# Performance work log

Hardware: AMD Instinct MI355X
Metric: run time of the kernel (lower is better)

Reference implementation:

```python
import jax, jax.numpy as jnp
import numpy as np

D = 256      # embedding_dim
DI = 512     # inner dim = proj_factor * D
H = 4        # num heads
DH = DI // H # head dim
L = 4        # num blocks
K = 4        # causal conv kernel size

def _ln(x, g, b):
    mu = jnp.mean(x, -1, keepdims=True)
    v = jnp.var(x, -1, keepdims=True)
    return (x - mu) * jax.lax.rsqrt(v + 1e-5) * g + b

def _causal_conv(x, w, b):
    # x [B,S,DI], w [K,DI] depthwise causal conv
    S = x.shape[1]
    xp = jnp.pad(x, ((0, 0), (K - 1, 0), (0, 0)))
    out = b
    for j in range(K):
        out = out + xp[:, j:j + S, :] * w[j]
    return out

def _mlstm(q, k, v, ip, fp):
    # parallel stabilized mLSTM. q,k,v [B,S,H,DH]; ip,fp [B,S,H]
    q = q.transpose(0, 2, 1, 3)
    k = k.transpose(0, 2, 1, 3)
    v = v.transpose(0, 2, 1, 3)
    ip = ip.transpose(0, 2, 1)  # [B,H,S]
    fp = fp.transpose(0, 2, 1)
    lf = jax.nn.log_sigmoid(fp)                      # log forget gates
    Fc = jnp.cumsum(lf, axis=-1)
    Fc = jnp.concatenate([jnp.zeros_like(Fc[..., :1]), Fc], axis=-1)  # [B,H,S+1]
    logfg = Fc[..., 1:, None] - Fc[..., None, 1:]    # [B,H,S,S]: sum of log f over (s,t]
    S_len = q.shape[2]
    tri = jnp.tril(jnp.ones((S_len, S_len), dtype=bool))
    logD = jnp.where(tri, logfg + ip[..., None, :], jnp.float32(-1e30))
    m = jnp.max(logD, axis=-1, keepdims=True)        # stabilizer
    Dm = jnp.exp(logD - m)
    qk = jnp.einsum('bhtd,bhsd->bhts', q, k) * (DH ** -0.5)
    C = qk * Dm
    norm = jnp.maximum(jnp.abs(jnp.sum(C, axis=-1, keepdims=True)), jnp.exp(-m))
    h = jnp.einsum('bhts,bhsd->bhtd', C / (norm + 1e-6), v)
    return h.transpose(0, 2, 1, 3)

def _forward(x, time_features, Wp, bp, ln_g, ln_b, Wup, bup, conv_w, conv_b,
             Wq, Wk, Wv, Wif, bif, gn_g, gn_b, skip, Wdown, bdown,
             lnf_g, lnf_b, Wf, bf):
    B, S = x.shape
    xi = jnp.concatenate([x[..., None], time_features], axis=-1)  # [B,S,5]
    h = xi @ Wp + bp                                              # [B,S,D]
    for l in range(L):
        res = h
        hn = _ln(h, ln_g[l], ln_b[l])
        up = hn @ Wup[l] + bup[l]                 # [B,S,2*DI]
        xm, z = up[..., :DI], up[..., DI:]
        xc = jax.nn.silu(_causal_conv(xm, conv_w[l], conv_b[l]))
        q = (xc @ Wq[l]).reshape(B, S, H, DH)
        k = (xc @ Wk[l]).reshape(B, S, H, DH)
        v = (xm @ Wv[l]).reshape(B, S, H, DH)
        gi = jnp.concatenate([q.reshape(B, S, DI), k.reshape(B, S, DI), v.reshape(B, S, DI)], axis=-1)
        gates = gi @ Wif[l] + bif[l]              # [B,S,2H]
        ht = _mlstm(q, k, v, gates[..., :H], gates[..., H:])  # [B,S,H,DH]
        ht = _ln(ht, gn_g[l].reshape(H, DH), gn_b[l].reshape(H, DH)).reshape(B, S, DI)
        ht = ht + skip[l] * xc
        ht = ht * jax.nn.silu(z)
        h = res + ht @ Wdown[l] + bdown[l]
    h = _ln(h, lnf_g, lnf_b)
    return h[:, -1, :] @ Wf + bf                  # [B,1]

def setup_inputs():
    key = jax.random.key(0)
    ks = jax.random.split(key, 16)
    B, S = 8, 1024
    sd = jnp.float32(0.02)
    return {
        'x': jax.random.normal(ks[0], (B, S), jnp.float32),
        'time_features': jax.random.normal(ks[1], (B, S, 4), jnp.float32),
        'Wp': jax.random.normal(ks[2], (5, D)) * sd, 'bp': jnp.zeros((D,)),
        'ln_g': jnp.ones((L, D)), 'ln_b': jnp.zeros((L, D)),
        'Wup': jax.random.normal(ks[3], (L, D, 2 * DI)) * sd, 'bup': jnp.zeros((L, 2 * DI)),
        'conv_w': jax.random.normal(ks[4], (L, K, DI)) * sd, 'conv_b': jnp.zeros((L, DI)),
        'Wq': jax.random.normal(ks[5], (L, DI, DI)) * sd,
        'Wk': jax.random.normal(ks[6], (L, DI, DI)) * sd,
        'Wv': jax.random.normal(ks[7], (L, DI, DI)) * sd,
        'Wif': jax.random.normal(ks[8], (L, 3 * DI, 2 * H)) * sd, 'bif': jnp.zeros((L, 2 * H)),
        'gn_g': jnp.ones((L, DI)), 'gn_b': jnp.zeros((L, DI)),
        'skip': jnp.ones((L, DI)),
        'Wdown': jax.random.normal(ks[9], (L, DI, D)) * sd, 'bdown': jnp.zeros((L, D)),
        'lnf_g': jnp.ones((D,)), 'lnf_b': jnp.zeros((D,)),
        'Wf': jax.random.normal(ks[10], (D, 1)) * sd, 'bf': jnp.zeros((1,)),
    }

def reference(x, time_features, Wp, bp, ln_g, ln_b, Wup, bup, conv_w, conv_b,
              Wq, Wk, Wv, Wif, bif, gn_g, gn_b, skip, Wdown, bdown,
              lnf_g, lnf_b, Wf, bf):
    return _forward(x, time_features, Wp, bp, ln_g, ln_b, Wup, bup, conv_w, conv_b,
                    Wq, Wk, Wv, Wif, bif, gn_g, gn_b, skip, Wdown, bdown,
                    lnf_g, lnf_b, Wf, bf)
```

## Files before the change

### kernel.cpp

```cpp
#include <hip/hip_runtime.h>
#include <hip/hip_bf16.h>
#include <math.h>

#define S 1024
#define NLAYER 4

typedef __bf16 bf16x8 __attribute__((ext_vector_type(8)));
typedef float floatx4 __attribute__((ext_vector_type(4)));

__device__ __forceinline__ float wave_sum(float v) {
  #pragma unroll
  for (int off = 32; off > 0; off >>= 1) v += __shfl_xor(v, off, 64);
  return v;
}

__device__ __forceinline__ void wtrans_body(
    int bid, const float* Wup, const float* Wq, const float* Wk, const float* Wv,
    const float* Wdown, __bf16* WupT, __bf16* WqkT, __bf16* WvT, __bf16* WdownT) {
  __shared__ float T[32][33];
  int layer = bid / 1152, rr = bid % 1152;
  const float* src; __bf16* dst; int K, N, tile;
  if (rr < 256)       { src = Wup   + layer * 262144; dst = WupT  + layer * 262144;          K = 256; N = 1024; tile = rr; }
  else if (rr < 512)  { src = Wq    + layer * 262144; dst = WqkT  + layer * 524288;          K = 512; N = 512;  tile = rr - 256; }
  else if (rr < 768)  { src = Wk    + layer * 262144; dst = WqkT  + layer * 524288 + 262144; K = 512; N = 512;  tile = rr - 512; }
  else if (rr < 1024) { src = Wv    + layer * 262144; dst = WvT   + layer * 262144;          K = 512; N = 512;  tile = rr - 768; }
  else                { src = Wdown + layer * 131072; dst = WdownT + layer * 131072;         K = 512; N = 256;  tile = rr - 1024; }
  int ntn = N >> 5;
  int tk = tile / ntn, tn = tile % ntn;
  int tid = threadIdx.x;
  int r = tid >> 3, c4 = (tid & 7) * 4;
  float4 v = *(const float4*)(src + (size_t)(tk * 32 + r) * N + tn * 32 + c4);
  T[c4 + 0][r] = v.x; T[c4 + 1][r] = v.y; T[c4 + 2][r] = v.z; T[c4 + 3][r] = v.w;
  __syncthreads();
  __bf16 o[4];
  #pragma unroll
  for (int j = 0; j < 4; ++j) o[j] = (__bf16)T[r][c4 + j];
  *(uint2*)(dst + (size_t)(tn * 32 + r) * K + tk * 32 + c4) = *(uint2*)o;
}

__device__ __forceinline__ void wgprep_body(
    int bid, const float* Wq, const float* Wk, const float* Wv,
    const float* Wif, float* wg) {
  int l = bid >> 8;
  int rem = bid & 255;
  int sel = rem >> 7;
  int kg = rem & 127;
  int tid = threadIdx.x;
  int wv = tid >> 6, lane = tid & 63;
  int k = kg * 4 + wv;
  const float* wif = Wif + (size_t)l * 1536 * 8;
  float part[8] = {0, 0, 0, 0, 0, 0, 0, 0};
  if (sel == 0) {
    const float* qr = Wq + (size_t)l * 262144 + (size_t)k * 512;
    const float* kr = Wk + (size_t)l * 262144 + (size_t)k * 512;
    #pragma unroll
    for (int i = 0; i < 8; ++i) {
      int n = lane + i * 64;
      float qv = qr[n], kv = kr[n];
      const float* wq8 = wif + (size_t)n * 8;
      const float* wk8 = wif + (size_t)(512 + n) * 8;
      #pragma unroll
      for (int j = 0; j < 8; ++j) part[j] += qv * wq8[j] + kv * wk8[j];
    }
  } else {
    const float* vr = Wv + (size_t)l * 262144 + (size_t)k * 512;
    #pragma unroll
    for (int i = 0; i < 8; ++i) {
      int n = lane + i * 64;
      float vv = vr[n];
      const float* wv8 = wif + (size_t)(1024 + n) * 8;
      #pragma unroll
      for (int j = 0; j < 8; ++j) part[j] += vv * wv8[j];
    }
  }
  #pragma unroll
  for (int j = 0; j < 8; ++j) part[j] = wave_sum(part[j]);
  if (lane < 8) wg[(size_t)l * 8192 + sel * 4096 + (size_t)k * 8 + lane] = part[lane];
}

__device__ __forceinline__ void embed_body(
    int row, const float* x, const float* tf, const float* Wp, const float* bp,
    const float* g, const float* b, float* h, __bf16* hn) {
  int n = threadIdx.x;
  float xv = x[row];
  const float* t4 = tf + (size_t)row * 4;
  float acc = bp[n] + xv * Wp[n];
  acc += t4[0] * Wp[256 + n];
  acc += t4[1] * Wp[512 + n];
  acc += t4[2] * Wp[768 + n];
  acc += t4[3] * Wp[1024 + n];
  h[(size_t)row * 256 + n] = acc;
  __shared__ float red[4];
  int wid = n >> 6, lane = n & 63;
  float s = wave_sum(acc);
  if (lane == 0) red[wid] = s;
  __syncthreads();
  float mu = (red[0] + red[1] + red[2] + red[3]) * (1.f / 256.f);
  __syncthreads();
  float d = acc - mu;
  float s2 = wave_sum(d * d);
  if (lane == 0) red[wid] = s2;
  __syncthreads();
  float var = (red[0] + red[1] + red[2] + red[3]) * (1.f / 256.f);
  float rs = rsqrtf(var + 1e-5f);
  hn[(size_t)row * 256 + n] = (__bf16)(d * rs * g[n] + b[n]);
}

__global__ __launch_bounds__(256) void prep_kernel(
    const float* __restrict__ x, const float* __restrict__ tf,
    const float* __restrict__ Wp, const float* __restrict__ bp,
    const float* __restrict__ ln_g, const float* __restrict__ ln_b,
    const float* __restrict__ Wup, const float* __restrict__ Wq,
    const float* __restrict__ Wk, const float* __restrict__ Wv,
    const float* __restrict__ Wdown, const float* __restrict__ Wif,
    __bf16* __restrict__ WupT, __bf16* __restrict__ WqkT,
    __bf16* __restrict__ WvT, __bf16* __restrict__ WdownT,
    float* __restrict__ wg, float* __restrict__ h, __bf16* __restrict__ hn) {
  int bid = blockIdx.x;
  if (bid < 4608) {
    wtrans_body(bid, Wup, Wq, Wk, Wv, Wdown, WupT, WqkT, WvT, WdownT);
  } else if (bid < 4608 + 1024) {
    wgprep_body(bid - 4608, Wq, Wk, Wv, Wif, wg);
  } else {
    embed_body(bid - 5632, x, tf, Wp, bp, ln_g, ln_b, h, hn);
  }
}

template <int TM, int MODE, int ACC>
__device__ __forceinline__ void hgemm_body(
    char* smem_raw,
    const __bf16* __restrict__ A, int lda,
    const __bf16* __restrict__ BT, int Kdim,
    const float* __restrict__ bias,
    void* __restrict__ Cout, int ldc, int bxi, int byi) {
  auto As = (__bf16(*)[40])smem_raw;
  auto Bs = (__bf16(*)[40])(smem_raw + (size_t)TM * 80);
  int tid = threadIdx.x;
  int bm = bxi * TM, bn = byi * 128;
  int wid = tid >> 6, lane = tid & 63;
  int wr = wid >> 1, wc = wid & 1;
  int lg = lane >> 4, li = lane & 15;
  constexpr int MI = TM / 32;
  constexpr int WROW = TM / 2;
  floatx4 acc[MI][4];
  #pragma unroll
  for (int i = 0; i < MI; ++i)
    #pragma unroll
    for (int j = 0; j < 4; ++j) acc[i][j] = (floatx4)(0.f);

  int arow = tid >> 2, aseg = tid & 3;
  bf16x8 pa0, pa1, pb0, pb1;
  auto pre = [&](int k0) {
    pa0 = *(const bf16x8*)(A + (size_t)(bm + arow) * lda + k0 + aseg * 8);
    if constexpr (TM == 128)
      pa1 = *(const bf16x8*)(A + (size_t)(bm + arow + 64) * lda + k0 + aseg * 8);
    pb0 = *(const bf16x8*)(BT + (size_t)(bn + arow) * Kdim + k0 + aseg * 8);
    pb1 = *(const bf16x8*)(BT + (size_t)(bn + arow + 64) * Kdim + k0 + aseg * 8);
  };
  pre(0);
  for (int k0 = 0; k0 < Kdim; k0 += 32) {
    __syncthreads();
    *(bf16x8*)&As[arow][aseg * 8] = pa0;
    if constexpr (TM == 128) *(bf16x8*)&As[arow + 64][aseg * 8] = pa1;
    *(bf16x8*)&Bs[arow][aseg * 8] = pb0;
    *(bf16x8*)&Bs[arow + 64][aseg * 8] = pb1;
    __syncthreads();
    if (k0 + 32 < Kdim) pre(k0 + 32);
    bf16x8 af[MI], bfr[4];
    #pragma unroll
    for (int mi = 0; mi < MI; ++mi)
      af[mi] = *(const bf16x8*)&As[wr * WROW + mi * 16 + li][lg * 8];
    #pragma unroll
    for (int ni = 0; ni < 4; ++ni)
      bfr[ni] = *(const bf16x8*)&Bs[wc * 64 + ni * 16 + li][lg * 8];
    #pragma unroll
    for (int mi = 0; mi < MI; ++mi)
      #pragma unroll
      for (int ni = 0; ni < 4; ++ni)
        acc[mi][ni] = __builtin_amdgcn_mfma_f32_16x16x32_bf16(af[mi], bfr[ni], acc[mi][ni], 0, 0, 0);
  }
  if constexpr (MODE == 1) {
    __bf16* eb = (__bf16*)smem_raw;
    const int PITCH = 136;
    __bf16* C = (__bf16*)Cout;
    #pragma unroll
    for (int mi = 0; mi < MI; ++mi) {
      __syncthreads();
      #pragma unroll
      for (int ni = 0; ni < 4; ++ni) {
        int col = wc * 64 + ni * 16 + li;
        float bz = bias ? bias[bn + col] : 0.f;
        #pragma unroll
        for (int r = 0; r < 4; ++r) {
          int lr = wr * 16 + lg * 4 + r;
          eb[lr * PITCH + col] = (__bf16)(acc[mi][ni][r] + bz);
        }
      }
      __syncthreads();
      #pragma unroll
      for (int i = 0; i < 2; ++i) {
        int lr = (tid >> 4) + i * 16;
        int c8 = (tid & 15) * 8;
        bf16x8 v = *(const bf16x8*)&eb[lr * PITCH + c8];
        int row_g = bm + (lr >> 4) * 64 + mi * 16 + (lr & 15);
        *(bf16x8*)(C + (size_t)row_g * ldc + bn + c8) = v;
      }
    }
  } else {
    #pragma unroll
    for (int mi = 0; mi < MI; ++mi) {
      int row = bm + wr * WROW + mi * 16 + lg * 4;
      #pragma unroll
      for (int ni = 0; ni < 4; ++ni) {
        int col = bn + wc * 64 + ni * 16 + li;
        if constexpr (MODE == 2) {
          __bf16 o4[4];
          #pragma unroll
          for (int r = 0; r < 4; ++r) o4[r] = (__bf16)acc[mi][ni][r];
          __bf16* vt = (__bf16*)Cout;
          size_t off = ((size_t)((row >> 10) * 4 + (col >> 7)) * 128 + (col & 127)) * 1024 + (row & 1023);
          *(uint2*)(vt + off) = *(uint2*)o4;
        } else {
          float bz = bias ? bias[col] : 0.f;
          float* C = (float*)Cout;
          #pragma unroll
          for (int r = 0; r < 4; ++r) {
            float v = acc[mi][ni][r] + bz;
            if (ACC) v += C[(size_t)(row + r) * ldc + col];
            C[(size_t)(row + r) * ldc + col] = v;
          }
        }
      }
    }
  }
}

template <int TM, int MODE, int ACC>
__global__ __launch_bounds__(256) void hgemm(
    const __bf16* __restrict__ A, int lda,
    const __bf16* __restrict__ BT, int Kdim,
    const float* __restrict__ bias,
    void* __restrict__ Cout, int ldc) {
  extern __shared__ char smem[];
  hgemm_body<TM, MODE, ACC>(smem, A, lda, BT, Kdim, bias, Cout, ldc,
                            blockIdx.x, blockIdx.y);
}

__global__ __launch_bounds__(256) void qkv_kernel(
    const __bf16* __restrict__ xc, const __bf16* __restrict__ WqkT,
    __bf16* __restrict__ qk, const __bf16* __restrict__ up,
    const __bf16* __restrict__ WvT, __bf16* __restrict__ vT) {
  extern __shared__ char smem[];
  if (blockIdx.y < 8) {
    hgemm_body<128, 1, 0>(smem, xc, 512, WqkT, 512, nullptr, qk, 1024,
                          blockIdx.x, blockIdx.y);
  } else {
    int j = blockIdx.y - 8;
    hgemm_body<64, 2, 0>(smem, up, 1024, WvT, 512, nullptr, vT, 0,
                         blockIdx.x * 2 + (j & 1), j >> 1);
  }
}

__global__ __launch_bounds__(256) void dgemm_ln_kernel(
    const __bf16* __restrict__ A, const __bf16* __restrict__ BT,
    const float* __restrict__ bias, float* __restrict__ h,
    const float* __restrict__ lng, const float* __restrict__ lnb,
    __bf16* __restrict__ hn) {
  __shared__ __bf16 As[32][40];
  __shared__ __bf16 Bs[256][40];
  __shared__ float redS[2][32], redQ[2][32];
  int tid = threadIdx.x;
  int bm = blockIdx.x * 32;
  int wid = tid >> 6, lane = tid & 63;
  int wr = wid >> 1, wc = wid & 1;
  int lg = lane >> 4, li = lane & 15;
  floatx4 acc[8];
  #pragma unroll
  for (int j = 0; j < 8; ++j) acc[j] = (floatx4)(0.f);

  int arow = tid >> 2, aseg = tid & 3;
  bf16x8 pa, pb[4];
  auto pre = [&](int k0) {
    if (tid < 128)
      pa = *(const bf16x8*)(A + (size_t)(bm + arow) * 512 + k0 + aseg * 8);
    #pragma unroll
    for (int i = 0; i < 4; ++i)
      pb[i] = *(const bf16x8*)(BT + (size_t)(arow + i * 64) * 512 + k0 + aseg * 8);
  };
  pre(0);
  for (int k0 = 0; k0 < 512; k0 += 32) {
    __syncthreads();
    if (tid < 128) *(bf16x8*)&As[arow][aseg * 8] = pa;
    #pragma unroll
    for (int i = 0; i < 4; ++i) *(bf16x8*)&Bs[arow + i * 64][aseg * 8] = pb[i];
    __syncthreads();
    if (k0 + 32 < 512) pre(k0 + 32);
    bf16x8 af = *(const bf16x8*)&As[wr * 16 + li][lg * 8];
    #pragma unroll
    for (int ni = 0; ni < 8; ++ni) {
      bf16x8 bfr = *(const bf16x8*)&Bs[wc * 128 + ni * 16 + li][lg * 8];
      acc[ni] = __builtin_amdgcn_mfma_f32_16x16x32_bf16(af, bfr, acc[ni], 0, 0, 0);
    }
  }
  #pragma unroll
  for (int r = 0; r < 4; ++r) {
    int lr = wr * 16 + lg * 4 + r;
    int row = bm + lr;
    float s1 = 0.f, s2 = 0.f;
    #pragma unroll
    for (int ni = 0; ni < 8; ++ni) {
      int col = wc * 128 + ni * 16 + li;
      float v = acc[ni][r] + bias[col] + h[(size_t)row * 256 + col];
      acc[ni][r] = v;
      h[(size_t)row * 256 + col] = v;
      s1 += v;
      s2 += v * v;
    }
    s1 += __shfl_xor(s1, 1, 64); s1 += __shfl_xor(s1, 2, 64);
    s1 += __shfl_xor(s1, 4, 64); s1 += __shfl_xor(s1, 8, 64);
    s2 += __shfl_xor(s2, 1, 64); s2 += __shfl_xor(s2, 2, 64);
    s2 += __shfl_xor(s2, 4, 64); s2 += __shfl_xor(s2, 8, 64);
    if (li == 0) { redS[wc][lr] = s1; redQ[wc][lr] = s2; }
  }
  if (!lng) return;
  __syncthreads();
  #pragma unroll
  for (int r = 0; r < 4; ++r) {
    int lr = wr * 16 + lg * 4 + r;
    int row = bm + lr;
    float s1 = redS[0][lr] + redS[1][lr];
    float s2 = redQ[0][lr] + redQ[1][lr];
    float mu = s1 * (1.f / 256.f);
    float var = s2 * (1.f / 256.f) - mu * mu;
    float rs = rsqrtf(var + 1e-5f);
    #pragma unroll
    for (int ni = 0; ni < 8; ++ni) {
      int col = wc * 128 + ni * 16 + li;
      hn[(size_t)row * 256 + col] = (__bf16)((acc[ni][r] - mu) * rs * lng[col] + lnb[col]);
    }
  }
}

__global__ __launch_bounds__(256) void conv_silu_kernel(
    const __bf16* __restrict__ up, const float* __restrict__ cw,
    const float* __restrict__ cb, const float* __restrict__ wg,
    const float* __restrict__ bif, __bf16* __restrict__ xc,
    float* __restrict__ gates) {
  int tid = threadIdx.x;
  int wv = tid >> 6, lane = tid & 63;
  int row = blockIdx.x * 4 + wv;
  int c8 = lane * 8;
  int t = row & (S - 1);
  float acc[8];
  *(float4*)&acc[0] = *(const float4*)(cb + c8);
  *(float4*)&acc[4] = *(const float4*)(cb + c8 + 4);
  float xm[8];
  #pragma unroll
  for (int j = 0; j < 4; ++j) {
    int tt = t - 3 + j;
    if (tt >= 0) {
      bf16x8 xv = *(const bf16x8*)(up + (size_t)(row - 3 + j) * 1024 + c8);
      float4 w0 = *(const float4*)(cw + j * 512 + c8);
      float4 w1 = *(const float4*)(cw + j * 512 + c8 + 4);
      acc[0] += w0.x * (float)xv[0]; acc[1] += w0.y * (float)xv[1];
      acc[2] += w0.z * (float)xv[2]; acc[3] += w0.w * (float)xv[3];
      acc[4] += w1.x * (float)xv[4]; acc[5] += w1.y * (float)xv[5];
      acc[6] += w1.z * (float)xv[6]; acc[7] += w1.w * (float)xv[7];
      if (j == 3) {
        #pragma unroll
        for (int m = 0; m < 8; ++m) xm[m] = (float)xv[m];
      }
    }
  }
  bf16x8 o;
  float xcs[8];
  #pragma unroll
  for (int m = 0; m < 8; ++m) {
    float sg = 1.f / (1.f + __expf(-acc[m]));
    xcs[m] = acc[m] * sg;
    o[m] = (__bf16)xcs[m];
  }
  *(bf16x8*)(xc + (size_t)row * 512 + c8) = o;
  const float* w1 = wg + (size_t)c8 * 8;
  const float* w2 = wg + 4096 + (size_t)c8 * 8;
  float part[8] = {0, 0, 0, 0, 0, 0, 0, 0};
  #pragma unroll
  for (int m = 0; m < 8; ++m) {
    const float* a = w1 + m * 8;
    const float* b = w2 + m * 8;
    #pragma unroll
    for (int j = 0; j < 8; ++j) part[j] += xcs[m] * a[j] + xm[m] * b[j];
  }
  #pragma unroll
  for (int j = 0; j < 8; ++j) part[j] = wave_sum(part[j]);
  if (lane < 8) gates[(size_t)row * 8 + lane] = part[lane] + bif[lane];
}

__global__ __launch_bounds__(64) void scan_kernel(
    const float* __restrict__ gates, float* __restrict__ gout,
    float* __restrict__ Mout, float* __restrict__ NFout) {
  int bh = blockIdx.x;
  int bb = bh >> 2, hh = bh & 3;
  int lane = threadIdx.x;
  float ip[16], pf[16];
  #pragma unroll
  for (int i = 0; i < 16; ++i) {
    int t = lane * 16 + i;
    const float* grow = gates + ((size_t)(bb * S + t)) * 8;
    ip[i] = grow[hh];
    float fp = grow[4 + hh];
    float lf = fminf(fp, 0.f) - log1pf(__expf(-fabsf(fp)));
    pf[i] = (i == 0) ? lf : pf[i - 1] + lf;
  }
  float T = pf[15];
  float inc = T;
  #pragma unroll
  for (int off = 1; off < 64; off <<= 1) {
    float v = __shfl_up(inc, off, 64);
    if (lane >= off) inc += v;
  }
  float excl = inc - T;
  float F[16], g[16], pm[16];
  #pragma unroll
  for (int i = 0; i < 16; ++i) {
    F[i] = excl + pf[i];
    g[i] = ip[i] - F[i];
    pm[i] = (i == 0) ? g[0] : fmaxf(pm[i - 1], g[i]);
  }
  float Mx = pm[15];
  float incm = Mx;
  #pragma unroll
  for (int off = 1; off < 64; off <<= 1) {
    float v = __shfl_up(incm, off, 64);
    if (lane >= off) incm = fmaxf(incm, v);
  }
  float em = __shfl_up(incm, 1, 64);
  if (lane == 0) em = -3.4e38f;
  #pragma unroll
  for (int i = 0; i < 16; ++i) {
    int t = lane * 16 + i;
    size_t o = (size_t)bh * S + t;
    float M = fmaxf(em, pm[i]);
    gout[o] = g[i];
    Mout[o] = M;
    NFout[o] = __expf(-F[i] - M);
  }
}

__global__ __launch_bounds__(256, 1) void attn_kernel(
    const __bf16* __restrict__ qk, const __bf16* __restrict__ vT,
    const float* __restrict__ gbuf, const float* __restrict__ Mbuf,
    const float* __restrict__ NFbuf,
    const float* __restrict__ gn_g, const float* __restrict__ gn_b,
    const float* __restrict__ skip,
    const __bf16* __restrict__ xc, const __bf16* __restrict__ up,
    __bf16* __restrict__ hd) {
  __shared__ __bf16 Ks[64][136];
  __shared__ __bf16 Vs[128][72];
  __shared__ __bf16 plds[4][2][16][72];
  __shared__ float gls[64];
  __shared__ float glds[128], blds[128], slds[128];
  int px = blockIdx.y, bh = blockIdx.x;
  int tqA = px, tqB = 15 - px;
  int bb = bh >> 2, hh = bh & 3;
  int tid = threadIdx.x;
  int wv = tid >> 6, lane = tid & 63;
  int lg = lane >> 4, li = lane & 15;
  int tbA = tqA * 64 + wv * 16;
  int tbB = tqB * 64 + wv * 16;
  const float scale = 0.08838834764831845f;

  if (tid < 128) {
    glds[tid] = gn_g[hh * 128 + tid];
    blds[tid] = gn_b[hh * 128 + tid];
    slds[tid] = skip[hh * 128 + tid];
  }

  bf16x8 aqA[4], aqB[4];
  {
    const __bf16* qpA = qk + ((size_t)(bb * S + tbA + li)) * 1024 + hh * 128 + lg * 8;
    const __bf16* qpB = qk + ((size_t)(bb * S + tbB + li)) * 1024 + hh * 128 + lg * 8;
    #pragma unroll
    for (int cd = 0; cd < 4; ++cd) {
      aqA[cd] = *(const bf16x8*)(qpA + cd * 32);
      aqB[cd] = *(const bf16x8*)(qpB + cd * 32);
    }
  }
  float mlA[4], nfA[4], mlB[4], nfB[4];
  #pragma unroll
  for (int r = 0; r < 4; ++r) {
    mlA[r] = Mbuf[(size_t)bh * S + tbA + lg * 4 + r];
    nfA[r] = NFbuf[(size_t)bh * S + tbA + lg * 4 + r];
    mlB[r] = Mbuf[(size_t)bh * S + tbB + lg * 4 + r];
    nfB[r] = NFbuf[(size_t)bh * S + tbB + lg * 4 + r];
  }

  floatx4 oA[8], oB[8];
  #pragma unroll
  for (int df = 0; df < 8; ++df) { oA[df] = (floatx4)(0.f); oB[df] = (floatx4)(0.f); }
  float rsA[4] = {0, 0, 0, 0}, rsB[4] = {0, 0, 0, 0};

  int krow = tid >> 3, kcol = tid & 7;
  bf16x8 kreg[4], vreg[4];
  float greg = 0.f;
  auto preload = [&](int st) {
    int s0 = st * 64;
    const __bf16* kp = qk + ((size_t)(bb * S + s0 + krow)) * 1024 + 512 + hh * 128;
    kreg[0] = *(const bf16x8*)(kp + kcol * 8);
    kreg[1] = *(const bf16x8*)(kp + (size_t)32 * 1024 + kcol * 8);
    kreg[2] = *(const bf16x8*)(kp + 64 + kcol * 8);
    kreg[3] = *(const bf16x8*)(kp + (size_t)32 * 1024 + 64 + kcol * 8);
    #pragma unroll
    for (int i = 0; i < 4; ++i)
      vreg[i] = *(const bf16x8*)(vT + ((size_t)(bh * 128 + krow + i * 32)) * 1024 + s0 + kcol * 8);
    if (tid < 64) greg = gbuf[(size_t)bh * S + s0 + tid];
  };
  preload(0);

  for (int st = 0; st <= tqB; ++st) {
    __syncthreads();
    *(bf16x8*)&Ks[krow][kcol * 8] = kreg[0];
    *(bf16x8*)&Ks[krow + 32][kcol * 8] = kreg[1];
    *(bf16x8*)&Ks[krow][64 + kcol * 8] = kreg[2];
    *(bf16x8*)&Ks[krow + 32][64 + kcol * 8] = kreg[3];
    #pragma unroll
    for (int i = 0; i < 4; ++i) *(bf16x8*)&Vs[krow + i * 32][kcol * 8] = vreg[i];
    if (tid < 64) gls[tid] = greg;
    __syncthreads();
    if (st < tqB) preload(st + 1);

    int s0 = st * 64;
    bool actA = (st <= tqA);
    #pragma unroll
    for (int ns = 0; ns < 4; ++ns) {
      bf16x8 bk0 = *(const bf16x8*)&Ks[ns * 16 + li][lg * 8];
      bf16x8 bk1 = *(const bf16x8*)&Ks[ns * 16 + li][32 + lg * 8];
      bf16x8 bk2 = *(const bf16x8*)&Ks[ns * 16 + li][64 + lg * 8];
      bf16x8 bk3 = *(const bf16x8*)&Ks[ns * 16 + li][96 + lg * 8];
      int s = s0 + ns * 16 + li;
      float gv = gls[ns * 16 + li];
      if (actA) {
        floatx4 pa = (floatx4)(0.f);
        pa = __builtin_amdgcn_mfma_f32_16x16x32_bf16(aqA[0], bk0, pa, 0, 0, 0);
        pa = __builtin_amdgcn_mfma_f32_16x16x32_bf16(aqA[1], bk1, pa, 0, 0, 0);
        pa = __builtin_amdgcn_mfma_f32_16x16x32_bf16(aqA[2], bk2, pa, 0, 0, 0);
        pa = __builtin_amdgcn_mfma_f32_16x16x32_bf16(aqA[3], bk3, pa, 0, 0, 0);
        #pragma unroll
        for (int r = 0; r < 4; ++r) {
          int t = tbA + lg * 4 + r;
          float val = pa[r] * scale * __expf(gv - mlA[r]);
          float w = (s <= t) ? val : 0.f;
          rsA[r] += w;
          plds[wv][0][lg * 4 + r][ns * 16 + li] = (__bf16)w;
        }
      }
      {
        floatx4 pb = (floatx4)(0.f);
        pb = __builtin_amdgcn_mfma_f32_16x16x32_bf16(aqB[0], bk0, pb, 0, 0, 0);
        pb = __builtin_amdgcn_mfma_f32_16x16x32_bf16(aqB[1], bk1, pb, 0, 0, 0);
        pb = __builtin_amdgcn_mfma_f32_16x16x32_bf16(aqB[2], bk2, pb, 0, 0, 0);
        pb = __builtin_amdgcn_mfma_f32_16x16x32_bf16(aqB[3], bk3, pb, 0, 0, 0);
        #pragma unroll
        for (int r = 0; r < 4; ++r) {
          int t = tbB + lg * 4 + r;
          float val = pb[r] * scale * __expf(gv - mlB[r]);
          float w = (s <= t) ? val : 0.f;
          rsB[r] += w;
          plds[wv][1][lg * 4 + r][ns * 16 + li] = (__bf16)w;
        }
      }
    }
    bf16x8 apA0, apA1, apB0, apB1;
    if (actA) {
      apA0 = *(const bf16x8*)&plds[wv][0][li][lg * 8];
      apA1 = *(const bf16x8*)&plds[wv][0][li][32 + lg * 8];
    }
    apB0 = *(const bf16x8*)&plds[wv][1][li][lg * 8];
    apB1 = *(const bf16x8*)&plds[wv][1][li][32 + lg * 8];
    #pragma unroll
    for (int df = 0; df < 8; ++df) {
      bf16x8 bv0 = *(const bf16x8*)&Vs[df * 16 + li][lg * 8];
      bf16x8 bv1 = *(const bf16x8*)&Vs[df * 16 + li][32 + lg * 8];
      if (actA) {
        oA[df] = __builtin_amdgcn_mfma_f32_16x16x32_bf16(apA0, bv0, oA[df], 0, 0, 0);
        oA[df] = __builtin_amdgcn_mfma_f32_16x16x32_bf16(apA1, bv1, oA[df], 0, 0, 0);
      }
      oB[df] = __builtin_amdgcn_mfma_f32_16x16x32_bf16(apB0, bv0, oB[df], 0, 0, 0);
      oB[df] = __builtin_amdgcn_mfma_f32_16x16x32_bf16(apB1, bv1, oB[df], 0, 0, 0);
    }
  }
  #pragma unroll
  for (int r = 0; r < 4; ++r) {
    float a = rsA[r], b = rsB[r];
    a += __shfl_xor(a, 1, 64); a += __shfl_xor(a, 2, 64);
    a += __shfl_xor(a, 4, 64); a += __shfl_xor(a, 8, 64);
    b += __shfl_xor(b, 1, 64); b += __shfl_xor(b, 2, 64);
    b += __shfl_xor(b, 4, 64); b += __shfl_xor(b, 8, 64);
    rsA[r] = a; rsB[r] = b;
  }
  #pragma unroll
  for (int tile = 0; tile < 2; ++tile) {
    int tb = tile == 0 ? tbA : tbB;
    #pragma unroll
    for (int r = 0; r < 4; ++r) {
      float rs = tile == 0 ? rsA[r] : rsB[r];
      float nf = tile == 0 ? nfA[r] : nfB[r];
      float inv = 1.f / (fmaxf(fabsf(rs), nf) + 1e-6f);
      float v8[8], s1 = 0.f, s2 = 0.f;
      #pragma unroll
      for (int df = 0; df < 8; ++df) {
        float v = (tile == 0 ? oA[df][r] : oB[df][r]) * inv;
        v8[df] = v;
        s1 += v;
        s2 += v * v;
      }
      s1 += __shfl_xor(s1, 1, 64); s1 += __shfl_xor(s1, 2, 64);
      s1 += __shfl_xor(s1, 4, 64); s1 += __shfl_xor(s1, 8, 64);
      s2 += __shfl_xor(s2, 1, 64); s2 += __shfl_xor(s2, 2, 64);
      s2 += __shfl_xor(s2, 4, 64); s2 += __shfl_xor(s2, 8, 64);
      float mu = s1 * (1.f / 128.f);
      float var = s2 * (1.f / 128.f) - mu * mu;
      float rq = rsqrtf(var + 1e-5f);
      int t = tb + lg * 4 + r;
      const __bf16* xr = xc + ((size_t)(bb * S + t)) * 512 + hh * 128 + li;
      const __bf16* zr = up + ((size_t)(bb * S + t)) * 1024 + 512 + hh * 128 + li;
      __bf16* od = hd + ((size_t)(bb * S + t)) * 512 + hh * 128 + li;
      #pragma unroll
      for (int df = 0; df < 8; ++df) {
        int c = df * 16 + li;
        float ln = (v8[df] - mu) * rq * glds[c] + blds[c];
        float val = ln + slds[c] * (float)xr[df * 16];
        float z = (float)zr[df * 16];
        float sg = 1.f / (1.f + __expf(-z));
        od[df * 16] = (__bf16)(val * (z * sg));
      }
    }
  }
}

__global__ __launch_bounds__(256) void final_kernel(
    const float* __restrict__ h, const float* __restrict__ g,
    const float* __restrict__ b, const float* __restrict__ Wf,
    const float* __restrict__ bf, float* __restrict__ out) {
  int bb = blockIdx.x, tid = threadIdx.x;
  size_t row = (size_t)(bb * S + S - 1) * 256;
  __shared__ float red[4];
  float v = h[row + tid];
  float s = wave_sum(v);
  int wid = tid >> 6, lane = tid & 63;
  if (lane == 0) red[wid] = s;
  __syncthreads();
  float mu = (red[0] + red[1] + red[2] + red[3]) * (1.f / 256.f);
  __syncthreads();
  float d = v - mu;
  float s2 = wave_sum(d * d);
  if (lane == 0) red[wid] = s2;
  __syncthreads();
  float var = (red[0] + red[1] + red[2] + red[3]) * (1.f / 256.f);
  float rs = rsqrtf(var + 1e-5f);
  float ln = d * rs * g[tid] + b[tid];
  float p = ln * Wf[tid];
  float psum = wave_sum(p);
  __syncthreads();
  if (lane == 0) red[wid] = psum;
  __syncthreads();
  if (tid == 0) out[bb] = red[0] + red[1] + red[2] + red[3] + bf[0];
}

extern "C" void kernel_launch(void* const* d_in, const int* in_sizes, int n_in,
                              void* d_out, int out_size, void* d_ws, size_t ws_size,
                              hipStream_t stream) {
  const float* x      = (const float*)d_in[0];
  const float* tf     = (const float*)d_in[1];
  const float* Wp     = (const float*)d_in[2];
  const float* bp     = (const float*)d_in[3];
  const float* ln_g   = (const float*)d_in[4];
  const float* ln_b   = (const float*)d_in[5];
  const float* Wup    = (const float*)d_in[6];
  const float* bup    = (const float*)d_in[7];
  const float* conv_w = (const float*)d_in[8];
  const float* conv_b = (const float*)d_in[9];
  const float* Wq     = (const float*)d_in[10];
  const float* Wk     = (const float*)d_in[11];
  const float* Wv     = (const float*)d_in[12];
  const float* Wif    = (const float*)d_in[13];
  const float* bif    = (const float*)d_in[14];
  const float* gn_g   = (const float*)d_in[15];
  const float* gn_b   = (const float*)d_in[16];
  const float* skip   = (const float*)d_in[17];
  const float* Wdown  = (const float*)d_in[18];
  const float* bdown  = (const float*)d_in[19];
  const float* lnf_g  = (const float*)d_in[20];
  const float* lnf_b  = (const float*)d_in[21];
  const float* Wf     = (const float*)d_in[22];
  const float* bf     = (const float*)d_in[23];
  float* out = (float*)d_out;

  float* h     = (float*)d_ws;
  float* gates = h + 2097152;
  float* gbuf  = gates + 65536;
  float* Mbuf  = gbuf + 32768;
  float* NFbuf = Mbuf + 32768;
  float* wgbuf = NFbuf + 32768;
  __bf16* hn   = (__bf16*)(wgbuf + 32768);
  __bf16* up   = hn + 2097152;
  __bf16* xc   = up + 8388608;
  __bf16* qk   = xc + 4194304;
  __bf16* vT   = qk + 8388608;
  __bf16* hd   = vT + 4194304;
  __bf16* WupT   = hd + 4194304;
  __bf16* WqkT   = WupT + 1048576;
  __bf16* WvT    = WqkT + 2097152;
  __bf16* WdownT = WvT + 1048576;

  prep_kernel<<<13824, 256, 0, stream>>>(
      x, tf, Wp, bp, ln_g, ln_b, Wup, Wq, Wk, Wv, Wdown, Wif,
      WupT, WqkT, WvT, WdownT, wgbuf, h, hn);
  for (int l = 0; l < NLAYER; ++l) {
    hgemm<128, 1, 0><<<dim3(64, 8), 256, 20480, stream>>>(
        hn, 256, WupT + (size_t)l * 262144, 256, bup + l * 1024, up, 1024);
    conv_silu_kernel<<<2048, 256, 0, stream>>>(up, conv_w + l * 2048, conv_b + l * 512,
                                               wgbuf + l * 8192, bif + l * 8, xc, gates);
    scan_kernel<<<32, 64, 0, stream>>>(gates, gbuf, Mbuf, NFbuf);
    qkv_kernel<<<dim3(64, 16), 256, 20480, stream>>>(
        xc, WqkT + (size_t)l * 524288, qk, up, WvT + (size_t)l * 262144, vT);
    attn_kernel<<<dim3(32, 8), 256, 0, stream>>>(
        qk, vT, gbuf, Mbuf, NFbuf, gn_g + l * 512, gn_b + l * 512, skip + l * 512,
        xc, up, hd);
    const float* lng = (l + 1 < NLAYER) ? (ln_g + (l + 1) * 256) : nullptr;
    const float* lnb = (l + 1 < NLAYER) ? (ln_b + (l + 1) * 256) : nullptr;
    dgemm_ln_kernel<<<256, 256, 0, stream>>>(
        hd, WdownT + (size_t)l * 131072, bdown + l * 256, h, lng, lnb, hn);
  }
  final_kernel<<<8, 256, 0, stream>>>(h, lnf_g, lnf_b, Wf, bf, out);
}
```

Baseline: 641.9 us.

## Fold scan into QKV launch and split attention query tiles across 512-thread blocks

The separate gate-scan kernel is removed and its work runs inside an extra row of blocks in the QKV GEMM launch, saving one launch per layer. The attention kernel moves to 512 threads so the two paired query tiles (front and back) are handled by separate groups of four waves instead of one wave computing both. This roughly halves per-wave accumulator registers and doubles the waves available to hide latency. The cost is idle waves for the shorter tile and a cooperative K/V load that now has to cover both tiles.

```diff
diff --git a/kernel.cpp b/kernel.cpp
--- a/kernel.cpp
+++ b/kernel.cpp
@@ -246,18 +246,72 @@
                             blockIdx.x, blockIdx.y);
 }
 
+__device__ __forceinline__ void scan_body(
+    int bh, int lane, const float* __restrict__ gates, float* __restrict__ gout,
+    float* __restrict__ Mout, float* __restrict__ NFout) {
+  int bb = bh >> 2, hh = bh & 3;
+  float ip[16], pf[16];
+  #pragma unroll
+  for (int i = 0; i < 16; ++i) {
+    int t = lane * 16 + i;
+    const float* grow = gates + ((size_t)(bb * S + t)) * 8;
+    ip[i] = grow[hh];
+    float fp = grow[4 + hh];
+    float lf = fminf(fp, 0.f) - log1pf(__expf(-fabsf(fp)));
+    pf[i] = (i == 0) ? lf : pf[i - 1] + lf;
+  }
+  float T = pf[15];
+  float inc = T;
+  #pragma unroll
+  for (int off = 1; off < 64; off <<= 1) {
+    float v = __shfl_up(inc, off, 64);
+    if (lane >= off) inc += v;
+  }
+  float excl = inc - T;
+  float F[16], g[16], pm[16];
+  #pragma unroll
+  for (int i = 0; i < 16; ++i) {
+    F[i] = excl + pf[i];
+    g[i] = ip[i] - F[i];
+    pm[i] = (i == 0) ? g[0] : fmaxf(pm[i - 1], g[i]);
+  }
+  float Mx = pm[15];
+  float incm = Mx;
+  #pragma unroll
+  for (int off = 1; off < 64; off <<= 1) {
+    float v = __shfl_up(incm, off, 64);
+    if (lane >= off) incm = fmaxf(incm, v);
+  }
+  float em = __shfl_up(incm, 1, 64);
+  if (lane == 0) em = -3.4e38f;
+  #pragma unroll
+  for (int i = 0; i < 16; ++i) {
+    int t = lane * 16 + i;
+    size_t o = (size_t)bh * S + t;
+    float M = fmaxf(em, pm[i]);
+    gout[o] = g[i];
+    Mout[o] = M;
+    NFout[o] = __expf(-F[i] - M);
+  }
+}
+
 __global__ __launch_bounds__(256) void qkv_kernel(
     const __bf16* __restrict__ xc, const __bf16* __restrict__ WqkT,
     __bf16* __restrict__ qk, const __bf16* __restrict__ up,
-    const __bf16* __restrict__ WvT, __bf16* __restrict__ vT) {
+    const __bf16* __restrict__ WvT, __bf16* __restrict__ vT,
+    const float* __restrict__ gates, float* __restrict__ gbuf,
+    float* __restrict__ Mbuf, float* __restrict__ NFbuf) {
   extern __shared__ char smem[];
   if (blockIdx.y < 8) {
     hgemm_body<128, 1, 0>(smem, xc, 512, WqkT, 512, nullptr, qk, 1024,
                           blockIdx.x, blockIdx.y);
-  } else {
+  } else if (blockIdx.y < 16) {
     int j = blockIdx.y - 8;
     hgemm_body<64, 2, 0>(smem, up, 1024, WvT, 512, nullptr, vT, 0,
                          blockIdx.x * 2 + (j & 1), j >> 1);
+  } else {
+    if (blockIdx.x < 32 && threadIdx.x < 64)
+      scan_body(blockIdx.x, threadIdx.x, gates, gbuf, Mbuf, NFbuf);
   }
 }
 
@@ -396,58 +450,7 @@
   if (lane < 8) gates[(size_t)row * 8 + lane] = part[lane] + bif[lane];
 }
 
-__global__ __launch_bounds__(64) void scan_kernel(
-    const float* __restrict__ gates, float* __restrict__ gout,
-    float* __restrict__ Mout, float* __restrict__ NFout) {
-  int bh = blockIdx.x;
-  int bb = bh >> 2, hh = bh & 3;
-  int lane = threadIdx.x;
-  float ip[16], pf[16];
-  #pragma unroll
-  for (int i = 0; i < 16; ++i) {
-    int t = lane * 16 + i;
-    const float* grow = gates + ((size_t)(bb * S + t)) * 8;
-    ip[i] = grow[hh];
-    float fp = grow[4 + hh];
-    float lf = fminf(fp, 0.f) - log1pf(__expf(-fabsf(fp)));
-    pf[i] = (i == 0) ? lf : pf[i - 1] + lf;
-  }
-  float T = pf[15];
-  float inc = T;
-  #pragma unroll
-  for (int off = 1; off < 64; off <<= 1) {
-    float v = __shfl_up(inc, off, 64);
-    if (lane >= off) inc += v;
-  }
-  float excl = inc - T;
-  float F[16], g[16], pm[16];
-  #pragma unroll
-  for (int i = 0; i < 16; ++i) {
-    F[i] = excl + pf[i];
-    g[i] = ip[i] - F[i];
-    pm[i] = (i == 0) ? g[0] : fmaxf(pm[i - 1], g[i]);
-  }
-  float Mx = pm[15];
-  float incm = Mx;
-  #pragma unroll
-  for (int off = 1; off < 64; off <<= 1) {
-    float v = __shfl_up(incm, off, 64);
-    if (lane >= off) incm = fmaxf(incm, v);
-  }
-  float em = __shfl_up(incm, 1, 64);
-  if (lane == 0) em = -3.4e38f;
-  #pragma unroll
-  for (int i = 0; i < 16; ++i) {
-    int t = lane * 16 + i;
-    size_t o = (size_t)bh * S + t;
-    float M = fmaxf(em, pm[i]);
-    gout[o] = g[i];
-    Mout[o] = M;
-    NFout[o] = __expf(-F[i] - M);
-  }
-}
-
-__global__ __launch_bounds__(256, 1) void attn_kernel(
+__global__ __launch_bounds__(512, 1) void attn_kernel(
     const __bf16* __restrict__ qk, const __bf16* __restrict__ vT,
     const float* __restrict__ gbuf, const float* __restrict__ Mbuf,
     const float* __restrict__ NFbuf,
@@ -457,7 +460,7 @@
     __bf16* __restrict__ hd) {
   __shared__ __bf16 Ks[64][136];
   __shared__ __bf16 Vs[128][72];
-  __shared__ __bf16 plds[4][2][16][72];
+  __shared__ __bf16 plds[8][16][72];
   __shared__ float gls[64];
   __shared__ float glds[128], blds[128], slds[128];
   int px = blockIdx.y, bh = blockIdx.x;
@@ -465,9 +468,10 @@
   int bb = bh >> 2, hh = bh & 3;
   int tid = threadIdx.x;
   int wv = tid >> 6, lane = tid & 63;
+  int sel = wv >> 2, wl = wv & 3;
   int lg = lane >> 4, li = lane & 15;
-  int tbA = tqA * 64 + wv * 16;
-  int tbB = tqB * 64 + wv * 16;
+  int tq = (sel == 0) ? tqA : tqB;
+  int tb = tq * 64 + wl * 16;
   const float scale = 0.08838834764831845f;
 
   if (tid < 128) {
@@ -476,164 +480,120 @@
     slds[tid] = skip[hh * 128 + tid];
   }
 
-  bf16x8 aqA[4], aqB[4];
+  bf16x8 aq[4];
   {
-    const __bf16* qpA = qk + ((size_t)(bb * S + tbA + li)) * 1024 + hh * 128 + lg * 8;
-    const __bf16* qpB = qk + ((size_t)(bb * S + tbB + li)) * 1024 + hh * 128 + lg * 8;
-    #pragma unroll
-    for (int cd = 0; cd < 4; ++cd) {
-      aqA[cd] = *(const bf16x8*)(qpA + cd * 32);
-      aqB[cd] = *(const bf16x8*)(qpB + cd * 32);
-    }
-  }
-  float mlA[4], nfA[4], mlB[4], nfB[4];
+    const __bf16* qp = qk + ((size_t)(bb * S + tb + li)) * 1024 + hh * 128 + lg * 8;
+    #pragma unroll
+    for (int cd = 0; cd < 4; ++cd) aq[cd] = *(const bf16x8*)(qp + cd * 32);
+  }
+  float ml[4], nf[4];
   #pragma unroll
   for (int r = 0; r < 4; ++r) {
-    mlA[r] = Mbuf[(size_t)bh * S + tbA + lg * 4 + r];
-    nfA[r] = NFbuf[(size_t)bh * S + tbA + lg * 4 + r];
-    mlB[r] = Mbuf[(size_t)bh * S + tbB + lg * 4 + r];
-    nfB[r] = NFbuf[(size_t)bh * S + tbB + lg * 4 + r];
-  }
-
-  floatx4 oA[8], oB[8];
-  #pragma unroll
-  for (int df = 0; df < 8; ++df) { oA[df] = (floatx4)(0.f); oB[df] = (floatx4)(0.f); }
-  float rsA[4] = {0, 0, 0, 0}, rsB[4] = {0, 0, 0, 0};
+    ml[r] = Mbuf[(size_t)bh * S + tb + lg * 4 + r];
+    nf[r] = NFbuf[(size_t)bh * S + tb + lg * 4 + r];
+  }
+
+  floatx4 oacc[8];
+  #pragma unroll
+  for (int df = 0; df < 8; ++df) oacc[df] = (floatx4)(0.f);
+  float rs[4] = {0, 0, 0, 0};
 
   int krow = tid >> 3, kcol = tid & 7;
-  bf16x8 kreg[4], vreg[4];
+  bf16x8 kreg0, kreg1, vreg0, vreg1;
   float greg = 0.f;
   auto preload = [&](int st) {
     int s0 = st * 64;
     const __bf16* kp = qk + ((size_t)(bb * S + s0 + krow)) * 1024 + 512 + hh * 128;
-    kreg[0] = *(const bf16x8*)(kp + kcol * 8);
-    kreg[1] = *(const bf16x8*)(kp + (size_t)32 * 1024 + kcol * 8);
-    kreg[2] = *(const bf16x8*)(kp + 64 + kcol * 8);
-    kreg[3] = *(const bf16x8*)(kp + (size_t)32 * 1024 + 64 + kcol * 8);
-    #pragma unroll
-    for (int i = 0; i < 4; ++i)
-      vreg[i] = *(const bf16x8*)(vT + ((size_t)(bh * 128 + krow + i * 32)) * 1024 + s0 + kcol * 8);
+    kreg0 = *(const bf16x8*)(kp + kcol * 8);
+    kreg1 = *(const bf16x8*)(kp + 64 + kcol * 8);
+    vreg0 = *(const bf16x8*)(vT + ((size_t)(bh * 128 + krow)) * 1024 + s0 + kcol * 8);
+    vreg1 = *(const bf16x8*)(vT + ((size_t)(bh * 128 + 64 + krow)) * 1024 + s0 + kcol * 8);
     if (tid < 64) greg = gbuf[(size_t)bh * S + s0 + tid];
   };
   preload(0);
 
   for (int st = 0; st <= tqB; ++st) {
     __syncthreads();
-    *(bf16x8*)&Ks[krow][kcol * 8] = kreg[0];
-    *(bf16x8*)&Ks[krow + 32][kcol * 8] = kreg[1];
-    *(bf16x8*)&Ks[krow][64 + kcol * 8] = kreg[2];
-    *(bf16x8*)&Ks[krow + 32][64 + kcol * 8] = kreg[3];
-    #pragma unroll
-    for (int i = 0; i < 4; ++i) *(bf16x8*)&Vs[krow + i * 32][kcol * 8] = vreg[i];
+    *(bf16x8*)&Ks[krow][kcol * 8] = kreg0;
+    *(bf16x8*)&Ks[krow][64 + kcol * 8] = kreg1;
+    *(bf16x8*)&Vs[krow][kcol * 8] = vreg0;
+    *(bf16x8*)&Vs[64 + krow][kcol * 8] = vreg1;
     if (tid < 64) gls[tid] = greg;
     __syncthreads();
     if (st < tqB) preload(st + 1);
 
-    int s0 = st * 64;
-    bool actA = (st <= tqA);
-    #pragma unroll
-    for (int ns = 0; ns < 4; ++ns) {
-      bf16x8 bk0 = *(const bf16x8*)&Ks[ns * 16 + li][lg * 8];
-      bf16x8 bk1 = *(const bf16x8*)&Ks[ns * 16 + li][32 + lg * 8];
-      bf16x8 bk2 = *(const bf16x8*)&Ks[ns * 16 + li][64 + lg * 8];
-      bf16x8 bk3 = *(const bf16x8*)&Ks[ns * 16 + li][96 + lg * 8];
-      int s = s0 + ns * 16 + li;
-      float gv = gls[ns * 16 + li];
-      if (actA) {
+    if (st <= tq) {
+      int s0 = st * 64;
+      #pragma unroll
+      for (int ns = 0; ns < 4; ++ns) {
+        bf16x8 bk0 = *(const bf16x8*)&Ks[ns * 16 + li][lg * 8];
+        bf16x8 bk1 = *(const bf16x8*)&Ks[ns * 16 + li][32 + lg * 8];
+        bf16x8 bk2 = *(const bf16x8*)&Ks[ns * 16 + li][64 + lg * 8];
+        bf16x8 bk3 = *(const bf16x8*)&Ks[ns * 16 + li][96 + lg * 8];
+        int s = s0 + ns * 16 + li;
+        float gv = gls[ns * 16 + li];
         floatx4 pa = (floatx4)(0.f);
-        pa = __builtin_amdgcn_mfma_f32_16x16x32_bf16(aqA[0], bk0, pa, 0, 0, 0);
-        pa = __builtin_amdgcn_mfma_f32_16x16x32_bf16(aqA[1], bk1, pa, 0, 0, 0);
-        pa = __builtin_amdgcn_mfma_f32_16x16x32_bf16(aqA[2], bk2, pa, 0, 0, 0);
-        pa = __builtin_amdgcn_mfma_f32_16x16x32_bf16(aqA[3], bk3, pa, 0, 0, 0);
+        pa = __builtin_amdgcn_mfma_f32_16x16x32_bf16(aq[0], bk0, pa, 0, 0, 0);
+        pa = __builtin_amdgcn_mfma_f32_16x16x32_bf16(aq[1], bk1, pa, 0, 0, 0);
+        pa = __builtin_amdgcn_mfma_f32_16x16x32_bf16(aq[2], bk2, pa, 0, 0, 0);
+        pa = __builtin_amdgcn_mfma_f32_16x16x32_bf16(aq[3], bk3, pa, 0, 0, 0);
         #pragma unroll
         for (int r = 0; r < 4; ++r) {
-          int t = tbA + lg * 4 + r;
-          float val = pa[r] * scale * __expf(gv - mlA[r]);
+          int t = tb + lg * 4 + r;
+          float val = pa[r] * scale * __expf(gv - ml[r]);
           float w = (s <= t) ? val : 0.f;
-          rsA[r] += w;
-          plds[wv][0][lg * 4 + r][ns * 16 + li] = (__bf16)w;
+          rs[r] += w;
+          plds[wv][lg * 4 + r][ns * 16 + li] = (__bf16)w;
         }
       }
-      {
-        floatx4 pb = (floatx4)(0.f);
-        pb = __builtin_amdgcn_mfma_f32_16x16x32_bf16(aqB[0], bk0, pb, 0, 0, 0);
-        pb = __builtin_amdgcn_mfma_f32_16x16x32_bf16(aqB[1], bk1, pb, 0, 0, 0);
-        pb = __builtin_amdgcn_mfma_f32_16x16x32_bf16(aqB[2], bk2, pb, 0, 0, 0);
-        pb = __builtin_amdgcn_mfma_f32_16x16x32_bf16(aqB[3], bk3, pb, 0, 0, 0);
-        #pragma unroll
-        for (int r = 0; r < 4; ++r) {
-          int t = tbB + lg * 4 + r;
-          float val = pb[r] * scale * __expf(gv - mlB[r]);
-          float w = (s <= t) ? val : 0.f;
-          rsB[r] += w;
-          plds[wv][1][lg * 4 + r][ns * 16 + li] = (__bf16)w;
-        }
+      bf16x8 ap0 = *(const bf16x8*)&plds[wv][li][lg * 8];
+      bf16x8 ap1 = *(const bf16x8*)&plds[wv][li][32 + lg * 8];
+      #pragma unroll
+      for (int df = 0; df < 8; ++df) {
+        bf16x8 bv0 = *(const bf16x8*)&Vs[df * 16 + li][lg * 8];
+        bf16x8 bv1 = *(const bf16x8*)&Vs[df * 16 + li][32 + lg * 8];
+        oacc[df] = __builtin_amdgcn_mfma_f32_16x16x32_bf16(ap0, bv0, oacc[df], 0, 0, 0);
+        oacc[df] = __builtin_amdgcn_mfma_f32_16x16x32_bf16(ap1, bv1, oacc[df], 0, 0, 0);
       }
     }
-    bf16x8 apA0, apA1, apB0, apB1;
-    if (actA) {
-      apA0 = *(const bf16x8*)&plds[wv][0][li][lg * 8];
-      apA1 = *(const bf16x8*)&plds[wv][0][li][32 + lg * 8];
-    }
-    apB0 = *(const bf16x8*)&plds[wv][1][li][lg * 8];
-    apB1 = *(const bf16x8*)&plds[wv][1][li][32 + lg * 8];
-    #pragma unroll
-    for (int df = 0; df < 8; ++df) {
-      bf16x8 bv0 = *(const bf16x8*)&Vs[df * 16 + li][lg * 8];
-      bf16x8 bv1 = *(const bf16x8*)&Vs[df * 16 + li][32 + lg * 8];
-      if (actA) {
-        oA[df] = __builtin_amdgcn_mfma_f32_16x16x32_bf16(apA0, bv0, oA[df], 0, 0, 0);
-        oA[df] = __builtin_amdgcn_mfma_f32_16x16x32_bf16(apA1, bv1, oA[df], 0, 0, 0);
-      }
-      oB[df] = __builtin_amdgcn_mfma_f32_16x16x32_bf16(apB0, bv0, oB[df], 0, 0, 0);
-      oB[df] = __builtin_amdgcn_mfma_f32_16x16x32_bf16(apB1, bv1, oB[df], 0, 0, 0);
-    }
   }
   #pragma unroll
   for (int r = 0; r < 4; ++r) {
-    float a = rsA[r], b = rsB[r];
+    float a = rs[r];
     a += __shfl_xor(a, 1, 64); a += __shfl_xor(a, 2, 64);
     a += __shfl_xor(a, 4, 64); a += __shfl_xor(a, 8, 64);
-    b += __shfl_xor(b, 1, 64); b += __shfl_xor(b, 2, 64);
-    b += __shfl_xor(b, 4, 64); b += __shfl_xor(b, 8, 64);
-    rsA[r] = a; rsB[r] = b;
-  }
-  #pragma unroll
-  for (int tile = 0; tile < 2; ++tile) {
-    int tb = tile == 0 ? tbA : tbB;
-    #pragma unroll
-    for (int r = 0; r < 4; ++r) {
-      float rs = tile == 0 ? rsA[r] : rsB[r];
-      float nf = tile == 0 ? nfA[r] : nfB[r];
-      float inv = 1.f / (fmaxf(fabsf(rs), nf) + 1e-6f);
-      float v8[8], s1 = 0.f, s2 = 0.f;
-      #pragma unroll
-      for (int df = 0; df < 8; ++df) {
-        float v = (tile == 0 ? oA[df][r] : oB[df][r]) * inv;
-        v8[df] = v;
-        s1 += v;
-        s2 += v * v;
-      }
-      s1 += __shfl_xor(s1, 1, 64); s1 += __shfl_xor(s1, 2, 64);
-      s1 += __shfl_xor(s1, 4, 64); s1 += __shfl_xor(s1, 8, 64);
-      s2 += __shfl_xor(s2, 1, 64); s2 += __shfl_xor(s2, 2, 64);
-      s2 += __shfl_xor(s2, 4, 64); s2 += __shfl_xor(s2, 8, 64);
-      float mu = s1 * (1.f / 128.f);
-      float var = s2 * (1.f / 128.f) - mu * mu;
-      float rq = rsqrtf(var + 1e-5f);
-      int t = tb + lg * 4 + r;
-      const __bf16* xr = xc + ((size_t)(bb * S + t)) * 512 + hh * 128 + li;
-      const __bf16* zr = up + ((size_t)(bb * S + t)) * 1024 + 512 + hh * 128 + li;
-      __bf16* od = hd + ((size_t)(bb * S + t)) * 512 + hh * 128 + li;
-      #pragma unroll
-      for (int df = 0; df < 8; ++df) {
-        int c = df * 16 + li;
-        float ln = (v8[df] - mu) * rq * glds[c] + blds[c];
-        float val = ln + slds[c] * (float)xr[df * 16];
-        float z = (float)zr[df * 16];
-        float sg = 1.f / (1.f + __expf(-z));
-        od[df * 16] = (__bf16)(val * (z * sg));
-      }
+    rs[r] = a;
+  }
+  #pragma unroll
+  for (int r = 0; r < 4; ++r) {
+    float inv = 1.f / (fmaxf(fabsf(rs[r]), nf[r]) + 1e-6f);
+    float v8[8], s1 = 0.f, s2 = 0.f;
+    #pragma unroll
+    for (int df = 0; df < 8; ++df) {
+      float v = oacc[df][r] * inv;
+      v8[df] = v;
+      s1 += v;
+      s2 += v * v;
+    }
+    s1 += __shfl_xor(s1, 1, 64); s1 += __shfl_xor(s1, 2, 64);
+    s1 += __shfl_xor(s1, 4, 64); s1 += __shfl_xor(s1, 8, 64);
+    s2 += __shfl_xor(s2, 1, 64); s2 += __shfl_xor(s2, 2, 64);
+    s2 += __shfl_xor(s2, 4, 64); s2 += __shfl_xor(s2, 8, 64);
+    float mu = s1 * (1.f / 128.f);
+    float var = s2 * (1.f / 128.f) - mu * mu;
+    float rq = rsqrtf(var + 1e-5f);
+    int t = tb + lg * 4 + r;
+    const __bf16* xr = xc + ((size_t)(bb * S + t)) * 512 + hh * 128 + li;
+    const __bf16* zr = up + ((size_t)(bb * S + t)) * 1024 + 512 + hh * 128 + li;
+    __bf16* od = hd + ((size_t)(bb * S + t)) * 512 + hh * 128 + li;
+    #pragma unroll
+    for (int df = 0; df < 8; ++df) {
+      int c = df * 16 + li;
+      float ln = (v8[df] - mu) * rq * glds[c] + blds[c];
+      float val = ln + slds[c] * (float)xr[df * 16];
+      float z = (float)zr[df * 16];
+      float sg = 1.f / (1.f + __expf(-z));
+      od[df * 16] = (__bf16)(val * (z * sg));
     }
   }
 }
@@ -721,10 +681,10 @@
         hn, 256, WupT + (size_t)l * 262144, 256, bup + l * 1024, up, 1024);
     conv_silu_kernel<<<2048, 256, 0, stream>>>(up, conv_w + l * 2048, conv_b + l * 512,
                                                wgbuf + l * 8192, bif + l * 8, xc, gates);
-    scan_kernel<<<32, 64, 0, stream>>>(gates, gbuf, Mbuf, NFbuf);
-    qkv_kernel<<<dim3(64, 16), 256, 20480, stream>>>(
-        xc, WqkT + (size_t)l * 524288, qk, up, WvT + (size_t)l * 262144, vT);
-    attn_kernel<<<dim3(32, 8), 256, 0, stream>>>(
+    qkv_kernel<<<dim3(64, 17), 256, 20480, stream>>>(
+        xc, WqkT + (size_t)l * 524288, qk, up, WvT + (size_t)l * 262144, vT,
+        gates, gbuf, Mbuf, NFbuf);
+    attn_kernel<<<dim3(32, 8), 512, 0, stream>>>(
         qk, vT, gbuf, Mbuf, NFbuf, gn_g + l * 512, gn_b + l * 512, skip + l * 512,
         xc, up, hd);
     const float* lng = (l + 1 < NLAYER) ? (ln_g + (l + 1) * 256) : nullptr;
```

Result: faster. 619.4 us (-3.5%).
